# Performance work log

Hardware: AMD Instinct MI355X
Metric: run time of the kernel (lower is better)

Reference implementation:

```python
import jax, jax.numpy as jnp
import numpy as np

K = 49        # k_neighbors
EPS = 1e-5    # BatchNorm2d eps


def setup_inputs() -> dict:
    key = jax.random.key(0)
    ks = jax.random.split(key, 2)
    B, C, M, O = 64, 64, 32, 128
    X = jax.random.normal(ks[0], (B, C, M, M), dtype=jnp.float32)
    # conv1x1 weight (kaiming fan_out) flattened to (O, C); bias init 0
    W = jax.random.normal(ks[1], (O, C), dtype=jnp.float32) * (2.0 / O) ** 0.5
    b = jnp.zeros((O,), jnp.float32)
    gamma = jnp.ones((O,), jnp.float32)
    beta = jnp.zeros((O,), jnp.float32)
    run_mean = jnp.zeros((O,), jnp.float32)
    run_var = jnp.ones((O,), jnp.float32)
    return dict(X=X, W=W, b=b, gamma=gamma, beta=beta,
                run_mean=run_mean, run_var=run_var)


def _knn_aggregate(x):
    """x: (N, C) node features -> D^{-1/2} A D^{-1/2} x for the kNN graph."""
    N = x.shape[0]
    sq = jnp.sum(x * x, axis=1)
    d2 = sq[:, None] + sq[None, :] - 2.0 * (x @ x.T)
    dist = jnp.sqrt(jnp.maximum(d2, 0.0))              # torch.cdist (p=2)
    i = jnp.arange(N)
    dist = dist.at[i, i].set(jnp.inf)                  # fill_diagonal_(inf)
    _, knn = jax.lax.top_k(-dist, K)                   # (N, K) nearest indices
    # topk indices are distinct -> every row degree == K, and the column
    # normalizer uses the col node's row degree (also K), so
    # D^{-1/2} A D^{-1/2} x == mean of gathered neighbors.
    nb = x[knn]                                        # (N, K, C) gather
    return nb.sum(axis=1) / K


def reference(X, W, b, gamma, beta, run_mean, run_var):
    B, C, M, _ = X.shape
    N = M * M
    x = X.reshape(B, C, N).transpose(0, 2, 1)          # (B, N, C) nodes
    Z = jax.vmap(_knn_aggregate)(x)                    # (B, N, C) sparse GCN agg
    # 1x1 conv over the (M, M) grid == per-node linear map
    Fg = jnp.einsum('oc,bnc->bon', W, Z) + b[None, :, None]   # (B, O, N)
    Fg = jax.nn.relu(Fg)
    # BatchNorm2d with running stats (eval mode); Dropout2d is identity in eval
    inv = jax.lax.rsqrt(run_var + EPS)
    Fg = gamma[None, :, None] * (Fg - run_mean[None, :, None]) * inv[None, :, None] + beta[None, :, None]
    return Fg.mean(axis=2)                             # AdaptiveAvgPool2d(1) -> (B, O)
```

## Files before the change

kernel.cpp:

```cpp
#include <hip/hip_runtime.h>
#include <stdint.h>

#define BATCH 64
#define CDIM  64
#define NPTS  1024
#define ODIM  128
#define KNN   49
#define KNNP  52
#define BNEPS 1e-5f

typedef __attribute__((ext_vector_type(8))) short bf16x8;
typedef __attribute__((ext_vector_type(4))) float f32x4;

__device__ __forceinline__ int mbcnt64(unsigned long long m) {
    return __builtin_amdgcn_mbcnt_hi((uint32_t)(m >> 32),
           __builtin_amdgcn_mbcnt_lo((uint32_t)m, 0));
}

#define O_XF   0
#define SZ_XF  (BATCH*64*2*64*8*4)
#define O_SQ   (O_XF + SZ_XF)
#define SZ_SQ  (BATCH*NPTS*4)
#define O_KNN  (O_SQ + SZ_SQ)
#define SZ_KNN (BATCH*NPTS*KNNP*4)
#define WS_NEED ((size_t)(O_KNN + SZ_KNN))

__global__ void gcn_init(const float* __restrict__ gamma, const float* __restrict__ beta,
                         const float* __restrict__ rmean, const float* __restrict__ rvar,
                         float* __restrict__ out) {
    int i = blockIdx.x * 256 + threadIdx.x;
    if (i < BATCH * ODIM) {
        int o = i & (ODIM - 1);
        out[i] = beta[o] - gamma[o] * rmean[o] * rsqrtf(rvar[o] + BNEPS);
    }
}

__global__ __launch_bounds__(256) void k0_split(const float* __restrict__ X,
                                                uint32_t* __restrict__ XF,
                                                float* __restrict__ sq,
                                                const float* __restrict__ gamma,
                                                const float* __restrict__ beta,
                                                const float* __restrict__ rmean,
                                                const float* __restrict__ rvar,
                                                float* __restrict__ out) {
    if (blockIdx.x < 32) {
        int i = blockIdx.x * 256 + threadIdx.x;
        int o = i & (ODIM - 1);
        out[i] = beta[o] - gamma[o] * rmean[o] * rsqrtf(rvar[o] + BNEPS);
    }
    const int b    = blockIdx.x >> 4;
    const int t16  = (blockIdx.x & 15) * 4 + (threadIdx.x >> 6);
    const int lane = threadIdx.x & 63;
    const int n    = t16 * 16 + (lane & 15);
    const int cg   = lane >> 4;
    const float* Xb = X + (size_t)b * CDIM * NPTS;
    float s = 0.f;
    for (int ks = 0; ks < 2; ks++) {
        uint32_t hi[4], lo[4];
#pragma unroll
        for (int dj = 0; dj < 4; dj++) {
            uint32_t hw[2], lw[2];
#pragma unroll
            for (int e = 0; e < 2; e++) {
                int c = ks * 32 + cg * 8 + dj * 2 + e;
                float x = Xb[(size_t)c * NPTS + n];
                s += x * x;
                uint32_t u  = __float_as_uint(x);
                uint32_t hr = (u + 0x7FFFu + ((u >> 16) & 1u)) >> 16;
                float    hf = __uint_as_float(hr << 16);
                uint32_t ul = __float_as_uint(x - hf);
                uint32_t lr = (ul + 0x7FFFu + ((ul >> 16) & 1u)) >> 16;
                hw[e] = hr; lw[e] = lr;
            }
            hi[dj] = hw[0] | (hw[1] << 16);
            lo[dj] = lw[0] | (lw[1] << 16);
        }
        size_t entry = ((size_t)(b * 64 + t16) * 2 + ks) * 64 + lane;
        uint32_t* p = XF + entry * 8;
        *(uint4*)p       = make_uint4(hi[0], hi[1], hi[2], hi[3]);
        *(uint4*)(p + 4) = make_uint4(lo[0], lo[1], lo[2], lo[3]);
    }
    s += __shfl_xor(s, 16, 64);
    s += __shfl_xor(s, 32, 64);
    if (lane < 16) sq[b * NPTS + n] = s;
}

__global__ __launch_bounds__(512) void k1_gram_select(const uint32_t* __restrict__ XF,
                                                      const float* __restrict__ sq,
                                                      int* __restrict__ knn) {
    __shared__ uint32_t s_pk[8 * 1024];
    const int b    = blockIdx.x >> 6;
    const int rt   = blockIdx.x & 63;
    const int wave = threadIdx.x >> 6, lane = threadIdx.x & 63;
    const int q = lane >> 4, l15 = lane & 15;
    int* eknn = (int*)s_pk;

    bf16x8 ahi[2], alo[2];
#pragma unroll
    for (int ks = 0; ks < 2; ks++) {
        const uint32_t* p = XF + (((size_t)(b * 64 + rt) * 2 + ks) * 64 + lane) * 8;
        ahi[ks] = *(const bf16x8*)p;
        alo[ks] = *(const bf16x8*)(p + 4);
    }
    const float* sqb = sq + b * NPTS;

#pragma unroll
    for (int tt = 0; tt < 8; tt++) {
        const int t16 = wave * 8 + tt;
        f32x4 acc = {0.f, 0.f, 0.f, 0.f};
#pragma unroll
        for (int ks = 0; ks < 2; ks++) {
            const uint32_t* p = XF + (((size_t)(b * 64 + t16) * 2 + ks) * 64 + lane) * 8;
            bf16x8 bhi = *(const bf16x8*)p;
            bf16x8 blo = *(const bf16x8*)(p + 4);
            acc = __builtin_amdgcn_mfma_f32_16x16x32_bf16(ahi[ks], bhi, acc, 0, 0, 0);
            acc = __builtin_amdgcn_mfma_f32_16x16x32_bf16(alo[ks], bhi, acc, 0, 0, 0);
            acc = __builtin_amdgcn_mfma_f32_16x16x32_bf16(ahi[ks], blo, acc, 0, 0, 0);
        }
        const int col  = t16 * 16 + l15;
        const float sqv = sqb[col];
        uint32_t k16[4];
#pragma unroll
        for (int i = 0; i < 4; i++) {
            int row = q * 4 + i;
            float d = fmaf(-2.f, acc[i], sqv);
            if (col == rt * 16 + row) d = __uint_as_float(0x7F800000u);
            uint32_t u = __float_as_uint(d);
            uint32_t key = ((int)u < 0) ? ~u : (u | 0x80000000u);
            k16[i] = key >> 16;
        }
        const int p0 = 2 * q, p1 = 2 * q + 1;
        s_pk[p0 * 1024 + (col ^ ((p0 & 3) << 3))] = k16[0] | (k16[1] << 16);
        s_pk[p1 * 1024 + (col ^ ((p1 & 3) << 3))] = k16[2] | (k16[3] << 16);
    }
    __syncthreads();

    uint32_t k0r[16], k1r[16];
    {
        const int sw = (wave & 3) << 3;
#pragma unroll
        for (int tt = 0; tt < 16; tt++) {
            uint32_t pk = s_pk[wave * 1024 + ((tt * 64 + lane) ^ sw)];
            k0r[tt] = pk & 0xFFFFu;
            k1r[tt] = pk >> 16;
        }
    }
    __syncthreads();
    if (threadIdx.x < 208) *(int4*)&eknn[threadIdx.x * 4] = make_int4(0, 0, 0, 0);

    uint32_t lo0, hi0, lo1, hi1;
    {
        uint32_t lm0 = k0r[0], lm1 = k1r[0];
#pragma unroll
        for (int tt = 1; tt < 16; tt++) {
            lm0 = k0r[tt] < lm0 ? k0r[tt] : lm0;
            lm1 = k1r[tt] < lm1 ? k1r[tt] : lm1;
        }
        uint32_t g0 = lm0, m0 = lm0, g1 = lm1, m1 = lm1;
#pragma unroll
        for (int off = 1; off < 64; off <<= 1) {
            uint32_t a0 = (uint32_t)__shfl_xor((int)g0, off, 64);
            uint32_t b0 = (uint32_t)__shfl_xor((int)m0, off, 64);
            uint32_t a1 = (uint32_t)__shfl_xor((int)g1, off, 64);
            uint32_t b1 = (uint32_t)__shfl_xor((int)m1, off, 64);
            g0 = a0 < g0 ? a0 : g0;  m0 = b0 > m0 ? b0 : m0;
            g1 = a1 < g1 ? a1 : g1;  m1 = b1 > m1 ? b1 : m1;
        }
        lo0 = g0; hi0 = m0;
        lo1 = g1; hi1 = m1;
    }

    for (int it = 0; it < 16; it++) {
        bool a0 = lo0 < hi0, a1 = lo1 < hi1;
        if (!a0 && !a1) break;
        uint32_t mid0 = (lo0 + hi0) >> 1;
        uint32_t mid1 = (lo1 + hi1) >> 1;
        int cnt0 = 0, cnt1 = 0;
#pragma unroll
        for (int tt = 0; tt < 16; tt++) {
            cnt0 += __popcll(__ballot(k0r[tt] <= mid0));
            cnt1 += __popcll(__ballot(k1r[tt] <= mid1));
        }
        if (a0) { if (cnt0 >= KNN) hi0 = mid0; else lo0 = mid0 + 1; }
        if (a1) { if (cnt1 >= KNN) hi1 = mid1; else lo1 = mid1 + 1; }
    }

#pragma unroll
    for (int r = 0; r < 2; r++) {
        const int row = wave * 2 + r;
        const uint32_t vstar = r ? lo1 : lo0;
        const uint32_t* k = r ? k1r : k0r;
        int total_lt = 0;
#pragma unroll
        for (int tt = 0; tt < 16; tt++)
            total_lt += __popcll(__ballot(k[tt] < vstar));
        int base_lt = 0, base_eq = total_lt;
#pragma unroll
        for (int tt = 0; tt < 16; tt++) {
            bool islt = k[tt] < vstar;
            bool iseq = k[tt] == vstar;
            unsigned long long mlt = __ballot(islt);
            unsigned long long meq = __ballot(iseq);
            if (mlt | meq) {
                int pos = islt ? (base_lt + mbcnt64(mlt)) : (base_eq + mbcnt64(meq));
                if (islt || (iseq && pos < KNN)) eknn[row * KNNP + pos] = tt * 64 + lane;
            }
            base_lt += __popcll(mlt);
            base_eq += __popcll(meq);
        }
    }
    __syncthreads();
    {
        const int t = threadIdx.x;
        int* kbase = knn + ((size_t)b * NPTS + rt * 16) * KNNP;
        if (t < 208) *(int4*)&kbase[t * 4] = *(const int4*)&eknn[t * 4];
    }
}

__global__ __launch_bounds__(256) void k2_fused(const float* __restrict__ X,
                                                const int* __restrict__ knn,
                                                const float* __restrict__ W,
                                                const float* __restrict__ bias,
                                                const float* __restrict__ gamma,
                                                const float* __restrict__ rvar,
                                                float* __restrict__ out) {
    __shared__ __align__(16) float XT8[8 * 1024];
    __shared__ float s_red[256];
    const int b = blockIdx.x >> 3, nq = blockIdx.x & 7;
    const int t = threadIdx.x;
    const int rl = t >> 1, gg = t & 1;
    const int row = nq * 128 + rl;
    const int* kr = knn + ((size_t)b * NPTS + row) * KNNP;
    int4 j[13];
#pragma unroll
    for (int c = 0; c < 13; c++) j[c] = *(const int4*)&kr[c * 4];

    float4 zacc[8];
    for (int cg8 = 0; cg8 < 8; cg8++) {
        __syncthreads();
        const float* Xc = X + ((size_t)b * CDIM + cg8 * 8) * NPTS;
#pragma unroll
        for (int k4 = 0; k4 < 4; k4++) {
            int n = k4 * 256 + t;
#pragma unroll
            for (int g2 = 0; g2 < 2; g2++) {
                float4 v;
                v.x = Xc[(size_t)(g2 * 4 + 0) * NPTS + n];
                v.y = Xc[(size_t)(g2 * 4 + 1) * NPTS + n];
                v.z = Xc[(size_t)(g2 * 4 + 2) * NPTS + n];
                v.w = Xc[(size_t)(g2 * 4 + 3) * NPTS + n];
                int sl = (g2 ^ (n & 1)) << 2;
                *(float4*)&XT8[n * 8 + sl] = v;
            }
        }
        __syncthreads();
        float4 s = {0.f, 0.f, 0.f, 0.f};
#pragma unroll
        for (int c = 0; c < 12; c++) {
            int js[4] = {j[c].x, j[c].y, j[c].z, j[c].w};
#pragma unroll
            for (int e = 0; e < 4; e++) {
                int jj = js[e];
                float4 v = *(const float4*)&XT8[jj * 8 + ((gg ^ (jj & 1)) << 2)];
                s.x += v.x; s.y += v.y; s.z += v.z; s.w += v.w;
            }
        }
        {
            int jj = j[12].x;
            float4 v = *(const float4*)&XT8[jj * 8 + ((gg ^ (jj & 1)) << 2)];
            s.x += v.x; s.y += v.y; s.z += v.z; s.w += v.w;
        }
        zacc[cg8] = s;
    }
    __syncthreads();
    float* ZT = XT8;
#pragma unroll
    for (int cg8 = 0; cg8 < 8; cg8++) {
        int colr = ((cg8 * 8 + gg * 4) + (rl & 15) * 4) & 63;
        *(float4*)&ZT[rl * 64 + colr] = zacc[cg8];
    }
    __syncthreads();

    const int o = t & 127, h = t >> 7;
    float4 wv[16];
#pragma unroll
    for (int c4 = 0; c4 < 16; c4++)
        wv[c4] = *(const float4*)&W[(size_t)o * CDIM + c4 * 4];
    const float bo = bias[o];
    float rsum = 0.f;
    for (int r = 0; r < 64; r++) {
        const int zr = h * 64 + r;
        const float* zrow = &ZT[zr * 64];
        const int rot = (zr & 15) * 4;
        float a = 0.f;
#pragma unroll
        for (int c4 = 0; c4 < 16; c4++) {
            float4 zv = *(const float4*)&zrow[(c4 * 4 + rot) & 63];
            a += wv[c4].x * zv.x + wv[c4].y * zv.y + wv[c4].z * zv.z + wv[c4].w * zv.w;
        }
        rsum += fmaxf(a * (1.f / KNN) + bo, 0.f);
    }
    s_red[t] = rsum;
    __syncthreads();
    if (t < 128) {
        float sum = s_red[t] + s_red[t + 128];
        float scale = gamma[t] * rsqrtf(rvar[t] + BNEPS) * (1.f / NPTS);
        atomicAdd(&out[b * ODIM + t], sum * scale);
    }
}

#define RTILE 8
#define APAD  1028
#define WPAD  132
#define POOLF (64 * WPAD)

__global__ __launch_bounds__(256) void gcn_main(
    const float* __restrict__ X, const float* __restrict__ W,
    const float* __restrict__ bias, const float* __restrict__ gamma,
    const float* __restrict__ rvar, float* __restrict__ out)
{
    __shared__ __align__(16) float s_pool[POOLF];
    __shared__ __align__(16) float s_fstage[4][APAD];
    __shared__ int   s_knn[RTILE][KNN];
    __shared__ float s_z[RTILE][CDIM];

    const int t = threadIdx.x;
    const int b = blockIdx.x >> 7;
    const int rtile = blockIdx.x & 127;
    const int r0 = rtile * RTILE;
    const float* Xb = X + (size_t)b * CDIM * NPTS;

    float acc[RTILE][4];
    float sqv[4];
#pragma unroll
    for (int r = 0; r < RTILE; r++)
#pragma unroll
        for (int u = 0; u < 4; u++) acc[r][u] = 0.f;
#pragma unroll
    for (int u = 0; u < 4; u++) sqv[u] = 0.f;

    for (int ch = 0; ch < 16; ch++) {
        const int c0 = ch * 4;
#pragma unroll
        for (int cc = 0; cc < 4; cc++) {
            float4 v = *(const float4*)(Xb + (size_t)(c0 + cc) * NPTS + 4 * t);
            *(float4*)&s_fstage[cc][4 * t] = v;
        }
        __syncthreads();
#pragma unroll
        for (int cc = 0; cc < 4; cc++) {
            float4 bv4 = *(const float4*)&s_fstage[cc][4 * t];
            float bv[4] = {bv4.x, bv4.y, bv4.z, bv4.w};
#pragma unroll
            for (int u = 0; u < 4; u++) sqv[u] += bv[u] * bv[u];
            const float* arow = Xb + (size_t)(c0 + cc) * NPTS + r0;
            float4 a0 = *(const float4*)(arow);
            float4 a1 = *(const float4*)(arow + 4);
            float av[8] = {a0.x, a0.y, a0.z, a0.w, a1.x, a1.y, a1.z, a1.w};
#pragma unroll
            for (int r = 0; r < RTILE; r++)
#pragma unroll
                for (int u = 0; u < 4; u++) acc[r][u] += av[r] * bv[u];
        }
        __syncthreads();
    }

    float* s_dist = s_pool;
#pragma unroll
    for (int r = 0; r < RTILE; r++) {
        const int rG = r0 + r;
        float d[4];
#pragma unroll
        for (int u = 0; u < 4; u++) {
            float dd = sqv[u] - 2.f * acc[r][u];
            d[u] = (4 * t + u == rG) ? __uint_as_float(0x7F800000u) : dd;
        }
        *(float4*)&s_dist[r * NPTS + 4 * t] = make_float4(d[0], d[1], d[2], d[3]);
    }
    __syncthreads();

    const int wave = t >> 6, lane = t & 63;
    const unsigned long long ltmask = (1ull << lane) - 1ull;
    for (int rr = 0; rr < 2; rr++) {
        const int row = wave * 2 + rr;
        unsigned key[16];
#pragma unroll
        for (int tt = 0; tt < 16; tt++) {
            unsigned u = __float_as_uint(s_dist[row * NPTS + tt * 64 + lane]);
            key[tt] = (u & 0x80000000u) ? ~u : (u | 0x80000000u);
        }
        unsigned lo = 0u, hi = 0xFFFFFFFFu;
        while (lo < hi) {
            unsigned mid = lo + ((hi - lo) >> 1);
            int cnt = 0;
#pragma unroll
            for (int tt = 0; tt < 16; tt++)
                cnt += __popcll(__ballot(key[tt] <= mid));
            if (cnt >= KNN) hi = mid; else lo = mid + 1;
        }
        const unsigned v49 = lo;
        int cntless = 0;
#pragma unroll
        for (int tt = 0; tt < 16; tt++)
            cntless += __popcll(__ballot(key[tt] < v49));
        const int need = KNN - cntless;
        int base = 0, eqtaken = 0;
#pragma unroll
        for (int tt = 0; tt < 16; tt++) {
            bool islt = key[tt] < v49;
            bool iseq = key[tt] == v49;
            unsigned long long meq = __ballot(iseq);
            int eqrank = eqtaken + __popcll(meq & ltmask);
            bool sel = islt || (iseq && (eqrank < need));
            unsigned long long msel = __ballot(sel);
            if (sel) {
                int pos = base + __popcll(msel & ltmask);
                s_knn[row][pos] = tt * 64 + lane;
            }
            base    += __popcll(msel);
            eqtaken += __popcll(meq);
        }
    }
    __syncthreads();

    float* astage = s_pool;
    float* s_redf = (float*)s_fstage;
    const int ar = t >> 5, acc8 = (t & 31) >> 2, ks = t & 3;
    for (int c0 = 0; c0 < CDIM; c0 += 8) {
#pragma unroll
        for (int qq = 0; qq < 8; qq++) {
            int if4 = qq * 256 + t;
            int cc = if4 >> 8, j4 = if4 & 255;
            float4 v = *(const float4*)(Xb + (size_t)(c0 + cc) * NPTS + 4 * j4);
            *(float4*)&astage[cc * APAD + 4 * j4] = v;
        }
        __syncthreads();
        float partial = 0.f;
        for (int k = ks; k < KNN; k += 4)
            partial += astage[acc8 * APAD + s_knn[ar][k]];
        s_redf[t] = partial;
        __syncthreads();
        if (t < 64) {
            int r = t >> 3, cc = t & 7;
            int bi = r * 32 + cc * 4;
            s_z[r][c0 + cc] = s_redf[bi] + s_redf[bi + 1] + s_redf[bi + 2] + s_redf[bi + 3];
        }
        __syncthreads();
    }

    float* wt = s_pool;
#pragma unroll 4
    for (int qq = 0; qq < 32; qq++) {
        int e = qq * 256 + t;
        int o = e >> 6, c = e & 63;
        wt[c * WPAD + o] = W[e];
    }
    __syncthreads();
    const int o = t & 127, rg = t >> 7;
    float facc[4] = {0.f, 0.f, 0.f, 0.f};
    for (int c = 0; c < CDIM; c += 4) {
        float w0 = wt[(c + 0) * WPAD + o], w1 = wt[(c + 1) * WPAD + o];
        float w2 = wt[(c + 2) * WPAD + o], w3 = wt[(c + 3) * WPAD + o];
#pragma unroll
        for (int qq = 0; qq < 4; qq++) {
            float4 zv = *(const float4*)&s_z[rg * 4 + qq][c];
            facc[qq] += w0 * zv.x + w1 * zv.y + w2 * zv.z + w3 * zv.w;
        }
    }
    const float bo = bias[o];
    float rsum = 0.f;
#pragma unroll
    for (int qq = 0; qq < 4; qq++) {
        float f = facc[qq] * (1.f / KNN) + bo;
        rsum += fmaxf(f, 0.f);
    }
    s_redf[t] = rsum;
    __syncthreads();
    if (t < 128) {
        float scale = gamma[t] * rsqrtf(rvar[t] + BNEPS) * (1.f / NPTS);
        atomicAdd(&out[b * ODIM + t], (s_redf[t] + s_redf[t + 128]) * scale);
    }
}

extern "C" void kernel_launch(void* const* d_in, const int* in_sizes, int n_in,
                              void* d_out, int out_size, void* d_ws, size_t ws_size,
                              hipStream_t stream) {
    const float* X     = (const float*)d_in[0];
    const float* W     = (const float*)d_in[1];
    const float* bias  = (const float*)d_in[2];
    const float* gamma = (const float*)d_in[3];
    const float* beta  = (const float*)d_in[4];
    const float* rmean = (const float*)d_in[5];
    const float* rvar  = (const float*)d_in[6];
    float* out = (float*)d_out;

    if (ws_size >= WS_NEED) {
        uint8_t* ws = (uint8_t*)d_ws;
        uint32_t* XF  = (uint32_t*)(ws + O_XF);
        float*    sqw = (float*)(ws + O_SQ);
        int*      knn = (int*)(ws + O_KNN);
        k0_split<<<BATCH * 16, 256, 0, stream>>>(X, XF, sqw, gamma, beta, rmean, rvar, out);
        k1_gram_select<<<BATCH * 64, 512, 0, stream>>>(XF, sqw, knn);
        k2_fused<<<BATCH * 8, 256, 0, stream>>>(X, knn, W, bias, gamma, rvar, out);
    } else {
        gcn_init<<<(BATCH * ODIM + 255) / 256, 256, 0, stream>>>(gamma, beta, rmean, rvar, out);
        gcn_main<<<BATCH * (NPTS / RTILE), 256, 0, stream>>>(X, W, bias, gamma, rvar, out);
    }
}
```

Before: 278.4 us.

## Use split-bf16 MFMA for conv epilogue and write kNN indices directly

The per-node 1x1 conv in the fused aggregation kernel moves from scalar FP32 dot products to bf16 MFMA. Both Z and W are split into hi/lo bf16 parts and combined with three MFMAs, which keeps close to FP32 accuracy while using the matrix cores. The kNN selection kernel now writes indices straight to global memory instead of staging them in LDS, dropping two block barriers, and it adds a minimum-blocks occupancy hint to its launch bounds. The trade-offs are some accuracy loss from dropping the lo*lo term and scattered, uncoalesced global stores of the indices.

```diff
diff --git a/kernel.cpp b/kernel.cpp
--- a/kernel.cpp
+++ b/kernel.cpp
@@ -8,13 +8,23 @@
 #define KNN   49
 #define KNNP  52
 #define BNEPS 1e-5f
+#define ZPAD  72
 
 typedef __attribute__((ext_vector_type(8))) short bf16x8;
 typedef __attribute__((ext_vector_type(4))) float f32x4;
+typedef union { bf16x8 v; uint32_t d[4]; } bfu;
 
 __device__ __forceinline__ int mbcnt64(unsigned long long m) {
     return __builtin_amdgcn_mbcnt_hi((uint32_t)(m >> 32),
            __builtin_amdgcn_mbcnt_lo((uint32_t)m, 0));
+}
+
+__device__ __forceinline__ void bf16_split(float x, uint32_t& h, uint32_t& l) {
+    uint32_t u = __float_as_uint(x);
+    h = (u + 0x7FFFu + ((u >> 16) & 1u)) >> 16;
+    float hf = __uint_as_float(h << 16);
+    uint32_t ul = __float_as_uint(x - hf);
+    l = (ul + 0x7FFFu + ((ul >> 16) & 1u)) >> 16;
 }
 
 #define O_XF   0
@@ -65,12 +75,7 @@
                 int c = ks * 32 + cg * 8 + dj * 2 + e;
                 float x = Xb[(size_t)c * NPTS + n];
                 s += x * x;
-                uint32_t u  = __float_as_uint(x);
-                uint32_t hr = (u + 0x7FFFu + ((u >> 16) & 1u)) >> 16;
-                float    hf = __uint_as_float(hr << 16);
-                uint32_t ul = __float_as_uint(x - hf);
-                uint32_t lr = (ul + 0x7FFFu + ((ul >> 16) & 1u)) >> 16;
-                hw[e] = hr; lw[e] = lr;
+                bf16_split(x, hw[e], lw[e]);
             }
             hi[dj] = hw[0] | (hw[1] << 16);
             lo[dj] = lw[0] | (lw[1] << 16);
@@ -85,15 +90,14 @@
     if (lane < 16) sq[b * NPTS + n] = s;
 }
 
-__global__ __launch_bounds__(512) void k1_gram_select(const uint32_t* __restrict__ XF,
-                                                      const float* __restrict__ sq,
-                                                      int* __restrict__ knn) {
+__global__ __launch_bounds__(512, 6) void k1_gram_select(const uint32_t* __restrict__ XF,
+                                                         const float* __restrict__ sq,
+                                                         int* __restrict__ knn) {
     __shared__ uint32_t s_pk[8 * 1024];
     const int b    = blockIdx.x >> 6;
     const int rt   = blockIdx.x & 63;
     const int wave = threadIdx.x >> 6, lane = threadIdx.x & 63;
     const int q = lane >> 4, l15 = lane & 15;
-    int* eknn = (int*)s_pk;
 
     bf16x8 ahi[2], alo[2];
 #pragma unroll
@@ -145,8 +149,6 @@
             k1r[tt] = pk >> 16;
         }
     }
-    __syncthreads();
-    if (threadIdx.x < 208) *(int4*)&eknn[threadIdx.x * 4] = make_int4(0, 0, 0, 0);
 
     uint32_t lo0, hi0, lo1, hi1;
     {
@@ -195,6 +197,7 @@
         for (int tt = 0; tt < 16; tt++)
             total_lt += __popcll(__ballot(k[tt] < vstar));
         int base_lt = 0, base_eq = total_lt;
+        int* kout = knn + ((size_t)b * NPTS + rt * 16 + row) * KNNP;
 #pragma unroll
         for (int tt = 0; tt < 16; tt++) {
             bool islt = k[tt] < vstar;
@@ -203,29 +206,27 @@
             unsigned long long meq = __ballot(iseq);
             if (mlt | meq) {
                 int pos = islt ? (base_lt + mbcnt64(mlt)) : (base_eq + mbcnt64(meq));
-                if (islt || (iseq && pos < KNN)) eknn[row * KNNP + pos] = tt * 64 + lane;
+                if (islt || (iseq && pos < KNN)) kout[pos] = tt * 64 + lane;
             }
             base_lt += __popcll(mlt);
             base_eq += __popcll(meq);
         }
     }
-    __syncthreads();
-    {
-        const int t = threadIdx.x;
-        int* kbase = knn + ((size_t)b * NPTS + rt * 16) * KNNP;
-        if (t < 208) *(int4*)&kbase[t * 4] = *(const int4*)&eknn[t * 4];
-    }
-}
-
-__global__ __launch_bounds__(256) void k2_fused(const float* __restrict__ X,
-                                                const int* __restrict__ knn,
-                                                const float* __restrict__ W,
-                                                const float* __restrict__ bias,
-                                                const float* __restrict__ gamma,
-                                                const float* __restrict__ rvar,
-                                                float* __restrict__ out) {
-    __shared__ __align__(16) float XT8[8 * 1024];
-    __shared__ float s_red[256];
+}
+
+__global__ __launch_bounds__(256) void k2_mfma(const float* __restrict__ X,
+                                               const int* __restrict__ knn,
+                                               const float* __restrict__ W,
+                                               const float* __restrict__ bias,
+                                               const float* __restrict__ gamma,
+                                               const float* __restrict__ rvar,
+                                               float* __restrict__ out) {
+    __shared__ __align__(16) uint32_t s_mem[(36864 + 2048) / 4];
+    float*    XT8 = (float*)s_mem;
+    uint16_t* ZFh = (uint16_t*)s_mem;
+    uint16_t* ZFl = ZFh + 128 * ZPAD;
+    float*    red = (float*)((uint8_t*)s_mem + 36864);
+
     const int b = blockIdx.x >> 3, nq = blockIdx.x & 7;
     const int t = threadIdx.x;
     const int rl = t >> 1, gg = t & 1;
@@ -273,39 +274,90 @@
         zacc[cg8] = s;
     }
     __syncthreads();
-    float* ZT = XT8;
+
 #pragma unroll
     for (int cg8 = 0; cg8 < 8; cg8++) {
-        int colr = ((cg8 * 8 + gg * 4) + (rl & 15) * 4) & 63;
-        *(float4*)&ZT[rl * 64 + colr] = zacc[cg8];
-    }
-    __syncthreads();
-
-    const int o = t & 127, h = t >> 7;
-    float4 wv[16];
-#pragma unroll
-    for (int c4 = 0; c4 < 16; c4++)
-        wv[c4] = *(const float4*)&W[(size_t)o * CDIM + c4 * 4];
-    const float bo = bias[o];
-    float rsum = 0.f;
-    for (int r = 0; r < 64; r++) {
-        const int zr = h * 64 + r;
-        const float* zrow = &ZT[zr * 64];
-        const int rot = (zr & 15) * 4;
-        float a = 0.f;
-#pragma unroll
-        for (int c4 = 0; c4 < 16; c4++) {
-            float4 zv = *(const float4*)&zrow[(c4 * 4 + rot) & 63];
-            a += wv[c4].x * zv.x + wv[c4].y * zv.y + wv[c4].z * zv.z + wv[c4].w * zv.w;
-        }
-        rsum += fmaxf(a * (1.f / KNN) + bo, 0.f);
-    }
-    s_red[t] = rsum;
+        const int c0 = cg8 * 8 + gg * 4;
+        float v[4] = {zacc[cg8].x, zacc[cg8].y, zacc[cg8].z, zacc[cg8].w};
+        uint32_t h[4], l[4];
+#pragma unroll
+        for (int e = 0; e < 4; e++) bf16_split(v[e], h[e], l[e]);
+        uint2 hd = make_uint2(h[0] | (h[1] << 16), h[2] | (h[3] << 16));
+        uint2 ld = make_uint2(l[0] | (l[1] << 16), l[2] | (l[3] << 16));
+        *(uint2*)&ZFh[rl * ZPAD + c0] = hd;
+        *(uint2*)&ZFl[rl * ZPAD + c0] = ld;
+    }
+    __syncthreads();
+
+    const int wave = t >> 6, lane = t & 63;
+    const int q = lane >> 4, l15 = lane & 15;
+    bf16x8 zah[2][2], zal[2][2];
+#pragma unroll
+    for (int m2 = 0; m2 < 2; m2++) {
+        const int m = (wave * 2 + m2) * 16 + l15;
+#pragma unroll
+        for (int kt = 0; kt < 2; kt++) {
+            const int kb = kt * 32 + q * 8;
+            zah[m2][kt] = *(const bf16x8*)&ZFh[m * ZPAD + kb];
+            zal[m2][kt] = *(const bf16x8*)&ZFl[m * ZPAD + kb];
+        }
+    }
+    const float inv49 = 1.f / KNN;
+    float p[8];
+#pragma unroll
+    for (int nt = 0; nt < 8; nt++) {
+        const int o = nt * 16 + l15;
+        bfu wh[2], wl[2];
+#pragma unroll
+        for (int kt = 0; kt < 2; kt++) {
+            const float* wp = W + (size_t)o * CDIM + kt * 32 + q * 8;
+            float4 wa = *(const float4*)wp;
+            float4 wb = *(const float4*)(wp + 4);
+            float wv[8] = {wa.x, wa.y, wa.z, wa.w, wb.x, wb.y, wb.z, wb.w};
+            uint32_t h[8], l[8];
+#pragma unroll
+            for (int e = 0; e < 8; e++) bf16_split(wv[e], h[e], l[e]);
+#pragma unroll
+            for (int dd = 0; dd < 4; dd++) {
+                wh[kt].d[dd] = h[2 * dd] | (h[2 * dd + 1] << 16);
+                wl[kt].d[dd] = l[2 * dd] | (l[2 * dd + 1] << 16);
+            }
+        }
+        f32x4 acc0 = {0.f, 0.f, 0.f, 0.f};
+        f32x4 acc1 = {0.f, 0.f, 0.f, 0.f};
+#pragma unroll
+        for (int kt = 0; kt < 2; kt++) {
+            acc0 = __builtin_amdgcn_mfma_f32_16x16x32_bf16(zah[0][kt], wh[kt].v, acc0, 0, 0, 0);
+            acc0 = __builtin_amdgcn_mfma_f32_16x16x32_bf16(zal[0][kt], wh[kt].v, acc0, 0, 0, 0);
+            acc0 = __builtin_amdgcn_mfma_f32_16x16x32_bf16(zah[0][kt], wl[kt].v, acc0, 0, 0, 0);
+            acc1 = __builtin_amdgcn_mfma_f32_16x16x32_bf16(zah[1][kt], wh[kt].v, acc1, 0, 0, 0);
+            acc1 = __builtin_amdgcn_mfma_f32_16x16x32_bf16(zal[1][kt], wh[kt].v, acc1, 0, 0, 0);
+            acc1 = __builtin_amdgcn_mfma_f32_16x16x32_bf16(zah[1][kt], wl[kt].v, acc1, 0, 0, 0);
+        }
+        const float bo = bias[o];
+        float s = 0.f;
+#pragma unroll
+        for (int reg = 0; reg < 4; reg++) {
+            s += fmaxf(fmaf(acc0[reg], inv49, bo), 0.f);
+            s += fmaxf(fmaf(acc1[reg], inv49, bo), 0.f);
+        }
+        p[nt] = s;
+    }
+#pragma unroll
+    for (int nt = 0; nt < 8; nt++) {
+        p[nt] += __shfl_xor(p[nt], 16, 64);
+        p[nt] += __shfl_xor(p[nt], 32, 64);
+    }
+    if (lane < 16) {
+#pragma unroll
+        for (int nt = 0; nt < 8; nt++)
+            red[wave * 128 + nt * 16 + l15] = p[nt];
+    }
     __syncthreads();
     if (t < 128) {
-        float sum = s_red[t] + s_red[t + 128];
+        float s = red[t] + red[128 + t] + red[256 + t] + red[384 + t];
         float scale = gamma[t] * rsqrtf(rvar[t] + BNEPS) * (1.f / NPTS);
-        atomicAdd(&out[b * ODIM + t], sum * scale);
+        atomicAdd(&out[b * ODIM + t], s * scale);
     }
 }
 
@@ -501,7 +553,7 @@
         int*      knn = (int*)(ws + O_KNN);
         k0_split<<<BATCH * 16, 256, 0, stream>>>(X, XF, sqw, gamma, beta, rmean, rvar, out);
         k1_gram_select<<<BATCH * 64, 512, 0, stream>>>(XF, sqw, knn);
-        k2_fused<<<BATCH * 8, 256, 0, stream>>>(X, knn, W, bias, gamma, rvar, out);
+        k2_mfma<<<BATCH * 8, 256, 0, stream>>>(X, knn, W, bias, gamma, rvar, out);
     } else {
         gcn_init<<<(BATCH * ODIM + 255) / 256, 256, 0, stream>>>(gamma, beta, rmean, rvar, out);
         gcn_main<<<BATCH * (NPTS / RTILE), 256, 0, stream>>>(X, W, bias, gamma, rvar, out);
```

Result: faster. 254.2 us (-8.7%).
